# Optimization experiments

Measured on AMD Instinct MI355X. Metric: run time of the kernel, lower is better.

The kernel has to match this reference:

```python
import jax, jax.numpy as jnp
import numpy as np

ALPHA = 32.0 ** 2
EPS = 1e-5
SCALE = 64 ** (-0.5)  # dim_head ** -0.5
HEADS = 8


def stable_softmax(t, alpha=ALPHA):
    t = t / alpha
    t = t - jax.lax.stop_gradient(jnp.max(t, axis=-1, keepdims=True))
    return jax.nn.softmax(t * alpha, axis=-1)


def setup_inputs() -> dict:
    key = jax.random.key(0)
    k1, k2, k3 = jax.random.split(key, 3)
    dim, inner = 512, 8 * 64
    x = jax.random.normal(k1, (8, dim, 32, 32), dtype=jnp.float32)
    gamma = jnp.ones((1, dim, 1, 1), dtype=jnp.float32)
    # conv2d 1x1 weights, stored as [out_ch, in_ch]
    w_qkv = jax.random.normal(k2, (inner * 3, dim), dtype=jnp.float32) * (dim ** -0.5)
    w_out = jax.random.normal(k3, (dim, inner), dtype=jnp.float32) * (inner ** -0.5)
    return {"x": x, "gamma": gamma, "w_qkv": w_qkv, "w_out": w_out}


def reference(x, gamma, w_qkv, w_out):
    b, c, H, W = x.shape
    residual = x
    # LayerNormChan: normalize over channel dim (biased variance), scale by gamma
    mean = jnp.mean(x, axis=1, keepdims=True)
    var = jnp.var(x, axis=1, keepdims=True)
    xn = (x - mean) / jnp.sqrt(var + EPS) * gamma
    # 1x1 conv QKV projection
    qkv = jnp.einsum('oc,bchw->bohw', w_qkv, xn)
    q, k, v = jnp.split(qkv, 3, axis=1)
    n = H * W
    def to_heads(t):
        return t.reshape(b, HEADS, -1, n)  # b h c (x y)
    q, k, v = map(to_heads, (q, k, v))
    sim = jnp.einsum('bhci,bhcj->bhij', q, k) * SCALE
    attn = stable_softmax(sim)
    out = jnp.einsum('bhij,bhcj->bhci', attn, v)
    out = out.reshape(b, -1, H, W)  # b (h c) x y
    out = jnp.einsum('oc,bchw->bohw', w_out, out)
    return out + residual
```

## Files before the change

kernel.cpp:

```cpp
#include <hip/hip_runtime.h>
#include <hip/hip_bf16.h>

#define NDIM   512
#define NPOS   1024
#define NB     8
#define INNER  1536
#define DHEAD  64

typedef __attribute__((ext_vector_type(8))) short bf8v;
typedef __attribute__((ext_vector_type(4))) float f4v;

__device__ __forceinline__ f4v mfma16(bf8v a, bf8v b, f4v c) {
    return __builtin_amdgcn_mfma_f32_16x16x32_bf16(a, b, c, 0, 0, 0);
}

__device__ __forceinline__ unsigned short f2bs(float v) {
    __hip_bfloat16 h = __float2bfloat16(v);
    return *reinterpret_cast<unsigned short*>(&h);
}

__device__ __forceinline__ void gl_lds16(const unsigned short* g, unsigned short* l) {
    __builtin_amdgcn_global_load_lds(
        (const __attribute__((address_space(1))) void*)g,
        (__attribute__((address_space(3))) void*)l,
        16, 0, 0);
}

__global__ __launch_bounds__(256) void ln_xnorm_kernel(
    const float* __restrict__ x, const float* __restrict__ gamma,
    unsigned short* __restrict__ xnT)
{
    __shared__ float ssum[4][64];
    __shared__ float ssq[4][64];
    __shared__ float mean_s[64];
    __shared__ float rstd_s[64];
    __shared__ unsigned short tile[64][72];

    const int b = blockIdx.y;
    const int n0 = blockIdx.x * 64;
    const int t = threadIdx.x;

    {
        const int ln = t & 63, cg = t >> 6;
        const float* xp = x + (size_t)b * NDIM * NPOS + n0 + ln;
        float s = 0.f, ss = 0.f;
        for (int c = cg * 128; c < cg * 128 + 128; ++c) {
            float v = xp[(size_t)c * NPOS];
            s += v; ss += v * v;
        }
        ssum[cg][ln] = s; ssq[cg][ln] = ss;
    }
    __syncthreads();
    if (t < 64) {
        float st = ssum[0][t] + ssum[1][t] + ssum[2][t] + ssum[3][t];
        float sq = ssq[0][t] + ssq[1][t] + ssq[2][t] + ssq[3][t];
        float m = st * (1.0f / NDIM);
        float var = sq * (1.0f / NDIM) - m * m;
        mean_s[t] = m;
        rstd_s[t] = rsqrtf(var + 1e-5f);
    }
    __syncthreads();

    const int cl = t >> 2, nq = (t & 3) * 16;
    const int n = t >> 2, cq = (t & 3) * 16;
    for (int c0 = 0; c0 < NDIM; c0 += 64) {
        const float g = gamma[c0 + cl];
        const float* xp = x + ((size_t)b * NDIM + c0 + cl) * NPOS + n0 + nq;
#pragma unroll
        for (int q = 0; q < 4; ++q) {
            float4 v = *(const float4*)(xp + q * 4);
            float4 m = *(const float4*)&mean_s[nq + q * 4];
            float4 r = *(const float4*)&rstd_s[nq + q * 4];
            tile[nq + q * 4 + 0][cl] = f2bs((v.x - m.x) * r.x * g);
            tile[nq + q * 4 + 1][cl] = f2bs((v.y - m.y) * r.y * g);
            tile[nq + q * 4 + 2][cl] = f2bs((v.z - m.z) * r.z * g);
            tile[nq + q * 4 + 3][cl] = f2bs((v.w - m.w) * r.w * g);
        }
        __syncthreads();
        unsigned short* dst = xnT + ((size_t)b * NPOS + n0 + n) * NDIM + c0 + cq;
        *(uint4*)dst       = *(const uint4*)&tile[n][cq];
        *(uint4*)(dst + 8) = *(const uint4*)&tile[n][cq + 8];
        __syncthreads();
    }
}

__global__ __launch_bounds__(256) void castw2_kernel(
    const float* __restrict__ wq, unsigned short* __restrict__ wqb,
    const float* __restrict__ wo, unsigned short* __restrict__ wob)
{
    const int n1 = INNER * NDIM / 4;
    int i = blockIdx.x * 256 + threadIdx.x;
    const float* src; unsigned short* dst; int j;
    if (i < n1) { src = wq; dst = wqb; j = i; }
    else        { src = wo; dst = wob; j = i - n1; }
    float4 v = ((const float4*)src)[j];
    ushort4 u;
    u.x = f2bs(v.x); u.y = f2bs(v.y); u.z = f2bs(v.z); u.w = f2bs(v.w);
    ((ushort4*)dst)[j] = u;
}

__global__ __launch_bounds__(256) void qkv_mfma_kernel(
    const unsigned short* __restrict__ wq, const unsigned short* __restrict__ xnT,
    unsigned short* __restrict__ qT, unsigned short* __restrict__ kT,
    unsigned short* __restrict__ vv)
{
    __shared__ __align__(16) unsigned short smem[4 * 64 * 72];
    unsigned short* At = smem;
    unsigned short* Bt = smem + 4096;

    const int b = blockIdx.z;
    const int m0 = blockIdx.y * 128, n0 = blockIdx.x * 128;
    const int t = threadIdx.x, w = t >> 6, lane = t & 63;
    const int l15 = lane & 15, quad = lane >> 4;
    const int wm = (w >> 1) * 64, wn = (w & 1) * 64;
    const unsigned short* Abase = wq + (size_t)m0 * NDIM;
    const unsigned short* Bbase = xnT + ((size_t)b * NPOS + n0) * NDIM;

    const int rl = lane >> 2, sl = lane & 3;
    const int cw = (sl ^ ((rl >> 1) & 3)) * 8;
    const int sA = (quad ^ ((l15 >> 1) & 3)) * 8;

    f4v acc[4][4];
#pragma unroll
    for (int i = 0; i < 4; ++i)
#pragma unroll
        for (int j = 0; j < 4; ++j) { acc[i][j][0]=0.f; acc[i][j][1]=0.f; acc[i][j][2]=0.f; acc[i][j][3]=0.f; }

    for (int k0 = 0; k0 < NDIM; k0 += 32) {
        __syncthreads();
#pragma unroll
        for (int e = 0; e < 2; ++e) {
            const int seg = w * 2 + e;
            const int r = seg * 16 + rl;
            gl_lds16(Abase + (size_t)r * NDIM + k0 + cw, At + seg * 512);
            gl_lds16(Bbase + (size_t)r * NDIM + k0 + cw, Bt + seg * 512);
        }
        __syncthreads();
        bf8v af[4], bfr[4];
#pragma unroll
        for (int ms = 0; ms < 4; ++ms) af[ms]  = *(const bf8v*)&At[(wm + ms * 16 + l15) * 32 + sA];
#pragma unroll
        for (int ns = 0; ns < 4; ++ns) bfr[ns] = *(const bf8v*)&Bt[(wn + ns * 16 + l15) * 32 + sA];
#pragma unroll
        for (int ms = 0; ms < 4; ++ms)
#pragma unroll
            for (int ns = 0; ns < 4; ++ns)
                acc[ms][ns] = mfma16(af[ms], bfr[ns], acc[ms][ns]);
    }
    __syncthreads();

    const int sec = m0 >> 9;
    const int om  = m0 & 511;
    if (sec == 2) {
        unsigned short* vbase = vv + ((size_t)b * NDIM + om) * NPOS + n0;
#pragma unroll
        for (int ms = 0; ms < 4; ++ms)
#pragma unroll
            for (int r = 0; r < 4; ++r) {
                int m = wm + ms * 16 + quad * 4 + r;
#pragma unroll
                for (int ns = 0; ns < 4; ++ns)
                    vbase[(size_t)m * NPOS + wn + ns * 16 + l15] = f2bs(acc[ms][ns][r]);
            }
    } else {
        const float qsc = (sec == 0) ? 0.125f : 1.0f;
        unsigned short* gT = (sec == 0 ? qT : kT) + ((size_t)b * NPOS + n0) * NDIM + om;
        unsigned short (*bw)[72] = (unsigned short(*)[72])(smem + w * 64 * 72);
#pragma unroll
        for (int ms = 0; ms < 4; ++ms)
#pragma unroll
            for (int ns = 0; ns < 4; ++ns)
#pragma unroll
                for (int r = 0; r < 4; ++r)
                    bw[ns * 16 + l15][ms * 16 + quad * 4 + r] = f2bs(acc[ms][ns][r] * qsc);
        unsigned short* dst = gT + (size_t)(wn + lane) * NDIM + wm;
#pragma unroll
        for (int q2 = 0; q2 < 8; ++q2)
            *(uint4*)(dst + q2 * 8) = *(const uint4*)&bw[lane][q2 * 8];
    }
}

__global__ __launch_bounds__(256, 2) void attn_mfma8_kernel(
    const unsigned short* __restrict__ qT, const unsigned short* __restrict__ kT,
    const unsigned short* __restrict__ vv, unsigned short* __restrict__ attnT)
{
    __shared__ __align__(16) unsigned short Kb[2][4096];
    __shared__ __align__(16) unsigned short Vb[2][4096];
    __shared__ __align__(16) unsigned short Ps[4][32][72];

    const int blk = blockIdx.x;
    const int xg = blk & 7, rr = blk >> 3;
    const int i0 = (rr & 7) * 128;
    const int bh = ((rr >> 3) << 3) | xg;
    const int b = bh >> 3, h = bh & 7;

    const int t = threadIdx.x, w = t >> 6, lane = t & 63;
    const int l15 = lane & 15, quad = lane >> 4;

    const unsigned short* kbase = kT + (size_t)b * NPOS * NDIM + h * DHEAD;
    const unsigned short* vbase = vv + ((size_t)b * NDIM + h * DHEAD) * NPOS;

    bf8v bq[2][2];
#pragma unroll
    for (int g = 0; g < 2; ++g) {
        const unsigned short* qrow =
            qT + ((size_t)b * NPOS + i0 + w * 32 + g * 16 + l15) * NDIM + h * DHEAD;
        bq[g][0] = *(const bf8v*)(qrow + quad * 8);
        bq[g][1] = *(const bf8v*)(qrow + 32 + quad * 8);
    }

    bf8v bones;
#pragma unroll
    for (int e = 0; e < 8; ++e) bones[e] = (short)0x3F80;

    const int rloc = lane >> 3;
    const int gch = ((lane & 7) ^ (rloc & 7)) * 8;

    const int sw0 = (quad ^ (l15 & 7)) * 8;
    const int sw1 = ((4 + quad) ^ (l15 & 7)) * 8;

#pragma unroll
    for (int e = 0; e < 2; ++e) {
        const int seg = w * 2 + e;
        const int row = seg * 8 + rloc;
        gl_lds16(kbase + (size_t)row * NDIM + gch, &Kb[0][seg * 512]);
        gl_lds16(vbase + (size_t)row * NPOS + gch, &Vb[0][seg * 512]);
    }

    f4v oc[2][5];
#pragma unroll
    for (int mg = 0; mg < 2; ++mg)
#pragma unroll
        for (int cs = 0; cs < 5; ++cs) { oc[mg][cs][0]=0.f; oc[mg][cs][1]=0.f; oc[mg][cs][2]=0.f; oc[mg][cs][3]=0.f; }

#pragma unroll 2
    for (int j0 = 0; j0 < NPOS; j0 += 64) {
        const int cur = (j0 >> 6) & 1, nxt = cur ^ 1;
        __syncthreads();
        if (j0 + 64 < NPOS) {
#pragma unroll
            for (int e = 0; e < 2; ++e) {
                const int seg = w * 2 + e;
                const int row = seg * 8 + rloc;
                gl_lds16(kbase + (size_t)(j0 + 64 + row) * NDIM + gch, &Kb[nxt][seg * 512]);
                gl_lds16(vbase + (size_t)row * NPOS + j0 + 64 + gch, &Vb[nxt][seg * 512]);
            }
        }

#pragma unroll
        for (int jt = 0; jt < 4; ++jt) {
            const int krow = (jt * 16 + l15) * 64;
            bf8v ak0 = *(const bf8v*)&Kb[cur][krow + sw0];
            bf8v ak1 = *(const bf8v*)&Kb[cur][krow + sw1];
#pragma unroll
            for (int g = 0; g < 2; ++g) {
                f4v s; s[0]=0.f; s[1]=0.f; s[2]=0.f; s[3]=0.f;
                s = mfma16(ak0, bq[g][0], s);
                s = mfma16(ak1, bq[g][1], s);
                ushort4 pu;
                pu.x = f2bs(__expf(fminf(s[0], 60.f)));
                pu.y = f2bs(__expf(fminf(s[1], 60.f)));
                pu.z = f2bs(__expf(fminf(s[2], 60.f)));
                pu.w = f2bs(__expf(fminf(s[3], 60.f)));
                *(ushort4*)&Ps[w][g * 16 + l15][jt * 16 + quad * 4] = pu;
            }
        }
        bf8v ap[2][2];
#pragma unroll
        for (int mg = 0; mg < 2; ++mg) {
            ap[mg][0] = *(const bf8v*)&Ps[w][mg * 16 + l15][quad * 8];
            ap[mg][1] = *(const bf8v*)&Ps[w][mg * 16 + l15][32 + quad * 8];
        }
#pragma unroll
        for (int cs = 0; cs < 4; ++cs) {
            const int vrow = (cs * 16 + l15) * 64;
            bf8v bv0 = *(const bf8v*)&Vb[cur][vrow + sw0];
            bf8v bv1 = *(const bf8v*)&Vb[cur][vrow + sw1];
#pragma unroll
            for (int mg = 0; mg < 2; ++mg) {
                oc[mg][cs] = mfma16(ap[mg][0], bv0, oc[mg][cs]);
                oc[mg][cs] = mfma16(ap[mg][1], bv1, oc[mg][cs]);
            }
        }
#pragma unroll
        for (int mg = 0; mg < 2; ++mg) {
            oc[mg][4] = mfma16(ap[mg][0], bones, oc[mg][4]);
            oc[mg][4] = mfma16(ap[mg][1], bones, oc[mg][4]);
        }
    }

#pragma unroll
    for (int mg = 0; mg < 2; ++mg) {
        float inv[4];
#pragma unroll
        for (int r = 0; r < 4; ++r) inv[r] = 1.0f / oc[mg][4][r];
        unsigned short* dst =
            attnT + ((size_t)b * NPOS + i0 + w * 32 + mg * 16) * NDIM + h * DHEAD;
#pragma unroll
        for (int cs = 0; cs < 4; ++cs)
#pragma unroll
            for (int r = 0; r < 4; ++r)
                dst[(size_t)(quad * 4 + r) * NDIM + cs * 16 + l15] = f2bs(oc[mg][cs][r] * inv[r]);
    }
}

__global__ __launch_bounds__(256) void out_mfma_kernel(
    const unsigned short* __restrict__ wo, const unsigned short* __restrict__ attnT,
    const float* __restrict__ x, float* __restrict__ outp)
{
    __shared__ __align__(16) unsigned short smem[6144];
    unsigned short* At = smem;
    unsigned short* Bt = smem + 2048;

    const int b = blockIdx.z;
    const int m0 = blockIdx.y * 64, n0 = blockIdx.x * 128;
    const int t = threadIdx.x, w = t >> 6, lane = t & 63;
    const int l15 = lane & 15, quad = lane >> 4;
    const int wm = (w >> 1) * 32, wn = (w & 1) * 64;
    const unsigned short* Abase = wo + (size_t)m0 * NDIM;
    const unsigned short* Bbase = attnT + ((size_t)b * NPOS + n0) * NDIM;

    const int rl = lane >> 2, sl = lane & 3;
    const int cw = (sl ^ ((rl >> 1) & 3)) * 8;
    const int sA = (quad ^ ((l15 >> 1) & 3)) * 8;

    f4v acc[2][4];
#pragma unroll
    for (int i = 0; i < 2; ++i)
#pragma unroll
        for (int j = 0; j < 4; ++j) { acc[i][j][0]=0.f; acc[i][j][1]=0.f; acc[i][j][2]=0.f; acc[i][j][3]=0.f; }

    for (int k0 = 0; k0 < NDIM; k0 += 32) {
        __syncthreads();
        {
            const int r = w * 16 + rl;
            gl_lds16(Abase + (size_t)r * NDIM + k0 + cw, At + w * 512);
        }
#pragma unroll
        for (int e = 0; e < 2; ++e) {
            const int seg = w * 2 + e;
            const int r = seg * 16 + rl;
            gl_lds16(Bbase + (size_t)r * NDIM + k0 + cw, Bt + seg * 512);
        }
        __syncthreads();
        bf8v af[2], bfr[4];
#pragma unroll
        for (int ms = 0; ms < 2; ++ms) af[ms]  = *(const bf8v*)&At[(wm + ms * 16 + l15) * 32 + sA];
#pragma unroll
        for (int ns = 0; ns < 4; ++ns) bfr[ns] = *(const bf8v*)&Bt[(wn + ns * 16 + l15) * 32 + sA];
#pragma unroll
        for (int ms = 0; ms < 2; ++ms)
#pragma unroll
            for (int ns = 0; ns < 4; ++ns)
                acc[ms][ns] = mfma16(af[ms], bfr[ns], acc[ms][ns]);
    }
    const float* xb = x + ((size_t)b * NDIM + m0) * NPOS + n0;
    float* ob = outp + ((size_t)b * NDIM + m0) * NPOS + n0;
#pragma unroll
    for (int ms = 0; ms < 2; ++ms)
#pragma unroll
        for (int r = 0; r < 4; ++r) {
            int m = wm + ms * 16 + quad * 4 + r;
#pragma unroll
            for (int ns = 0; ns < 4; ++ns) {
                int n = wn + ns * 16 + l15;
                ob[(size_t)m * NPOS + n] = acc[ms][ns][r] + xb[(size_t)m * NPOS + n];
            }
        }
}

extern "C" void kernel_launch(void* const* d_in, const int* in_sizes, int n_in,
                              void* d_out, int out_size, void* d_ws, size_t ws_size,
                              hipStream_t stream) {
    const float* x     = (const float*)d_in[0];
    const float* gamma = (const float*)d_in[1];
    const float* w_qkv = (const float*)d_in[2];
    const float* w_out = (const float*)d_in[3];
    float* out = (float*)d_out;

    unsigned short* xnT = (unsigned short*)d_ws;
    unsigned short* wqb = xnT + (size_t)NB * NPOS * NDIM;
    unsigned short* wob = wqb + (size_t)INNER * NDIM;
    unsigned short* qTw = wob + (size_t)NDIM * NDIM;
    unsigned short* kTw = qTw + (size_t)NB * NPOS * NDIM;
    unsigned short* vvw = kTw + (size_t)NB * NPOS * NDIM;
    unsigned short* aTw = vvw + (size_t)NB * NPOS * NDIM;

    ln_xnorm_kernel<<<dim3(NPOS / 64, NB), 256, 0, stream>>>(x, gamma, xnT);
    castw2_kernel<<<(INNER * NDIM + NDIM * NDIM) / 4 / 256, 256, 0, stream>>>(
        w_qkv, wqb, w_out, wob);
    qkv_mfma_kernel<<<dim3(NPOS / 128, INNER / 128, NB), 256, 0, stream>>>(
        wqb, xnT, qTw, kTw, vvw);
    attn_mfma8_kernel<<<512, 256, 0, stream>>>(qTw, kTw, vvw, aTw);
    out_mfma_kernel<<<dim3(NPOS / 128, NDIM / 64, NB), 256, 0, stream>>>(wob, aTw, x, out);
}
```

Before: 151.9 us.

## Double-buffer LDS in projection GEMMs and merge prep kernels into one launch

Merges the layer-norm/transpose kernel and the weight-cast kernel into one launch, split by block index, to save a launch and let the two run concurrently. Both the QKV and output-projection GEMMs now double-buffer their LDS tiles: the next K-slice is issued with global_load_lds before computing on the current one, and one barrier per iteration is dropped. This aims to hide global-to-LDS latency behind MFMA work. The risk is that, with the second barrier gone, nothing explicitly waits for the other waves' async LDS writes to land before reads, so correctness depends on compiler-inserted waits. Those waits could also serialize the loads and cancel the overlap.

New measurement: 146.0 us. 3.9% less time.

```diff
diff --git a/kernel.cpp b/kernel.cpp
--- a/kernel.cpp
+++ b/kernel.cpp
@@ -26,20 +26,34 @@
         16, 0, 0);
 }
 
-__global__ __launch_bounds__(256) void ln_xnorm_kernel(
+__global__ __launch_bounds__(256) void prep_kernel(
     const float* __restrict__ x, const float* __restrict__ gamma,
-    unsigned short* __restrict__ xnT)
+    const float* __restrict__ wq, const float* __restrict__ wo,
+    unsigned short* __restrict__ xnT, unsigned short* __restrict__ wqb,
+    unsigned short* __restrict__ wob)
 {
+    const int blk = blockIdx.x;
+    const int t = threadIdx.x;
+    if (blk >= 128) {
+        const int n1 = INNER * NDIM / 4;
+        int i = (blk - 128) * 256 + t;
+        const float* src; unsigned short* dst; int j;
+        if (i < n1) { src = wq; dst = wqb; j = i; }
+        else        { src = wo; dst = wob; j = i - n1; }
+        float4 v = ((const float4*)src)[j];
+        ushort4 u;
+        u.x = f2bs(v.x); u.y = f2bs(v.y); u.z = f2bs(v.z); u.w = f2bs(v.w);
+        ((ushort4*)dst)[j] = u;
+        return;
+    }
     __shared__ float ssum[4][64];
     __shared__ float ssq[4][64];
     __shared__ float mean_s[64];
     __shared__ float rstd_s[64];
     __shared__ unsigned short tile[64][72];
 
-    const int b = blockIdx.y;
-    const int n0 = blockIdx.x * 64;
-    const int t = threadIdx.x;
-
+    const int b = blk >> 4;
+    const int n0 = (blk & 15) * 64;
     {
         const int ln = t & 63, cg = t >> 6;
         const float* xp = x + (size_t)b * NDIM * NPOS + n0 + ln;
@@ -84,29 +98,12 @@
     }
 }
 
-__global__ __launch_bounds__(256) void castw2_kernel(
-    const float* __restrict__ wq, unsigned short* __restrict__ wqb,
-    const float* __restrict__ wo, unsigned short* __restrict__ wob)
-{
-    const int n1 = INNER * NDIM / 4;
-    int i = blockIdx.x * 256 + threadIdx.x;
-    const float* src; unsigned short* dst; int j;
-    if (i < n1) { src = wq; dst = wqb; j = i; }
-    else        { src = wo; dst = wob; j = i - n1; }
-    float4 v = ((const float4*)src)[j];
-    ushort4 u;
-    u.x = f2bs(v.x); u.y = f2bs(v.y); u.z = f2bs(v.z); u.w = f2bs(v.w);
-    ((ushort4*)dst)[j] = u;
-}
-
 __global__ __launch_bounds__(256) void qkv_mfma_kernel(
     const unsigned short* __restrict__ wq, const unsigned short* __restrict__ xnT,
     unsigned short* __restrict__ qT, unsigned short* __restrict__ kT,
     unsigned short* __restrict__ vv)
 {
     __shared__ __align__(16) unsigned short smem[4 * 64 * 72];
-    unsigned short* At = smem;
-    unsigned short* Bt = smem + 4096;
 
     const int b = blockIdx.z;
     const int m0 = blockIdx.y * 128, n0 = blockIdx.x * 128;
@@ -126,16 +123,29 @@
 #pragma unroll
         for (int j = 0; j < 4; ++j) { acc[i][j][0]=0.f; acc[i][j][1]=0.f; acc[i][j][2]=0.f; acc[i][j][3]=0.f; }
 
+#pragma unroll
+    for (int e = 0; e < 2; ++e) {
+        const int seg = w * 2 + e;
+        const int r = seg * 16 + rl;
+        gl_lds16(Abase + (size_t)r * NDIM + cw, smem + seg * 512);
+        gl_lds16(Bbase + (size_t)r * NDIM + cw, smem + 4096 + seg * 512);
+    }
+
     for (int k0 = 0; k0 < NDIM; k0 += 32) {
+        const int cur = (k0 >> 5) & 1;
+        unsigned short* At = smem + cur * 8192;
+        unsigned short* Bt = At + 4096;
         __syncthreads();
-#pragma unroll
-        for (int e = 0; e < 2; ++e) {
-            const int seg = w * 2 + e;
-            const int r = seg * 16 + rl;
-            gl_lds16(Abase + (size_t)r * NDIM + k0 + cw, At + seg * 512);
-            gl_lds16(Bbase + (size_t)r * NDIM + k0 + cw, Bt + seg * 512);
-        }
-        __syncthreads();
+        if (k0 + 32 < NDIM) {
+            unsigned short* An = smem + (cur ^ 1) * 8192;
+#pragma unroll
+            for (int e = 0; e < 2; ++e) {
+                const int seg = w * 2 + e;
+                const int r = seg * 16 + rl;
+                gl_lds16(Abase + (size_t)r * NDIM + k0 + 32 + cw, An + seg * 512);
+                gl_lds16(Bbase + (size_t)r * NDIM + k0 + 32 + cw, An + 4096 + seg * 512);
+            }
+        }
         bf8v af[4], bfr[4];
 #pragma unroll
         for (int ms = 0; ms < 4; ++ms) af[ms]  = *(const bf8v*)&At[(wm + ms * 16 + l15) * 32 + sA];
@@ -215,7 +225,6 @@
 
     const int rloc = lane >> 3;
     const int gch = ((lane & 7) ^ (rloc & 7)) * 8;
-
     const int sw0 = (quad ^ (l15 & 7)) * 8;
     const int sw1 = ((4 + quad) ^ (l15 & 7)) * 8;
 
@@ -308,9 +317,7 @@
     const unsigned short* __restrict__ wo, const unsigned short* __restrict__ attnT,
     const float* __restrict__ x, float* __restrict__ outp)
 {
-    __shared__ __align__(16) unsigned short smem[6144];
-    unsigned short* At = smem;
-    unsigned short* Bt = smem + 2048;
+    __shared__ __align__(16) unsigned short smem[12288];
 
     const int b = blockIdx.z;
     const int m0 = blockIdx.y * 64, n0 = blockIdx.x * 128;
@@ -330,19 +337,33 @@
 #pragma unroll
         for (int j = 0; j < 4; ++j) { acc[i][j][0]=0.f; acc[i][j][1]=0.f; acc[i][j][2]=0.f; acc[i][j][3]=0.f; }
 
-    for (int k0 = 0; k0 < NDIM; k0 += 32) {
-        __syncthreads();
-        {
-            const int r = w * 16 + rl;
-            gl_lds16(Abase + (size_t)r * NDIM + k0 + cw, At + w * 512);
-        }
+    {
+        const int r = w * 16 + rl;
+        gl_lds16(Abase + (size_t)r * NDIM + cw, smem + w * 512);
 #pragma unroll
         for (int e = 0; e < 2; ++e) {
             const int seg = w * 2 + e;
-            const int r = seg * 16 + rl;
-            gl_lds16(Bbase + (size_t)r * NDIM + k0 + cw, Bt + seg * 512);
-        }
+            const int rb = seg * 16 + rl;
+            gl_lds16(Bbase + (size_t)rb * NDIM + cw, smem + 2048 + seg * 512);
+        }
+    }
+
+    for (int k0 = 0; k0 < NDIM; k0 += 32) {
+        const int cur = (k0 >> 5) & 1;
+        unsigned short* At = smem + cur * 6144;
+        unsigned short* Bt = At + 2048;
         __syncthreads();
+        if (k0 + 32 < NDIM) {
+            unsigned short* An = smem + (cur ^ 1) * 6144;
+            const int r = w * 16 + rl;
+            gl_lds16(Abase + (size_t)r * NDIM + k0 + 32 + cw, An + w * 512);
+#pragma unroll
+            for (int e = 0; e < 2; ++e) {
+                const int seg = w * 2 + e;
+                const int rb = seg * 16 + rl;
+                gl_lds16(Bbase + (size_t)rb * NDIM + k0 + 32 + cw, An + 2048 + seg * 512);
+            }
+        }
         bf8v af[2], bfr[4];
 #pragma unroll
         for (int ms = 0; ms < 2; ++ms) af[ms]  = *(const bf8v*)&At[(wm + ms * 16 + l15) * 32 + sA];
@@ -386,9 +407,8 @@
     unsigned short* vvw = kTw + (size_t)NB * NPOS * NDIM;
     unsigned short* aTw = vvw + (size_t)NB * NPOS * NDIM;
 
-    ln_xnorm_kernel<<<dim3(NPOS / 64, NB), 256, 0, stream>>>(x, gamma, xnT);
-    castw2_kernel<<<(INNER * NDIM + NDIM * NDIM) / 4 / 256, 256, 0, stream>>>(
-        w_qkv, wqb, w_out, wob);
+    prep_kernel<<<128 + (INNER * NDIM + NDIM * NDIM) / 4 / 256, 256, 0, stream>>>(
+        x, gamma, w_qkv, w_out, xnT, wqb, wob);
     qkv_mfma_kernel<<<dim3(NPOS / 128, INNER / 128, NB), 256, 0, stream>>>(
         wqb, xnT, qTw, kTw, vvw);
     attn_mfma8_kernel<<<512, 256, 0, stream>>>(qTw, kTw, vvw, aTw);
```
